# Performance work log

Hardware: AMD Instinct MI355X
Metric: run time of the kernel (lower is better)

Reference implementation:

```python
import jax, jax.numpy as jnp
import numpy as np

V, F_IN, H, DH, T = 512, 8, 64, 4, 3
E, P, L = 8192, 64, 8
D = H + DH  # path-decoder GRU width


def setup_inputs() -> dict:
    key = jax.random.key(0)
    ks = jax.random.split(key, 24)
    s = 0.1
    inp = {
        "adj_matrix": jax.random.normal(ks[0], (V, V, F_IN), jnp.float32),
        "edges": jax.random.randint(ks[1], (E, 2), 0, V),
        "paths": jax.random.randint(ks[2], (P, L), 0, V),
        "demands": jax.random.uniform(ks[3], (P,), jnp.float32),
        "emb_w": jax.random.normal(ks[4], (H, F_IN), jnp.float32) * s,
        "w1s": jax.random.normal(ks[5], (T, H, H), jnp.float32) * s,
        "w2s": jax.random.normal(ks[6], (T, H, H), jnp.float32) * s,
        "w3s": jax.random.normal(ks[7], (T, H, H), jnp.float32) * s,
        "gru_w_ih": jax.random.normal(ks[8], (3 * H, 2 * H), jnp.float32) * s,
        "gru_w_hh": jax.random.normal(ks[9], (3 * H, H), jnp.float32) * s,
        "gru_b_ih": jax.random.normal(ks[10], (3 * H,), jnp.float32) * s,
        "gru_b_hh": jax.random.normal(ks[11], (3 * H,), jnp.float32) * s,
        "pf_w_ih": jax.random.normal(ks[12], (3 * D, D), jnp.float32) * s,
        "pf_w_hh": jax.random.normal(ks[13], (3 * D, D), jnp.float32) * s,
        "pf_b_ih": jax.random.normal(ks[14], (3 * D,), jnp.float32) * s,
        "pf_b_hh": jax.random.normal(ks[15], (3 * D,), jnp.float32) * s,
        "pb_w_ih": jax.random.normal(ks[16], (3 * D, D), jnp.float32) * s,
        "pb_w_hh": jax.random.normal(ks[17], (3 * D, D), jnp.float32) * s,
        "pb_b_ih": jax.random.normal(ks[18], (3 * D,), jnp.float32) * s,
        "pb_b_hh": jax.random.normal(ks[19], (3 * D,), jnp.float32) * s,
        "wq": jax.random.normal(ks[20], (1, D), jnp.float32) * s,
        "bq": jax.random.normal(ks[21], (1,), jnp.float32) * s,
        "wd": jax.random.normal(ks[22], (DH, 1), jnp.float32) * s,
    }
    return inp


def _gru(x_seq, h0, w_ih, w_hh, b_ih, b_hh):
    """torch-style GRU, batch_first. x_seq (B,Tn,I), h0 (B,Hd) -> (ys, h_last)."""
    def step(h, x_t):
        gi = x_t @ w_ih.T + b_ih
        gh = h @ w_hh.T + b_hh
        ir, iz, inn = jnp.split(gi, 3, axis=-1)
        hr, hz, hn = jnp.split(gh, 3, axis=-1)
        r = jax.nn.sigmoid(ir + hr)
        z = jax.nn.sigmoid(iz + hz)
        n = jnp.tanh(inn + r * hn)
        h_new = (1.0 - z) * n + z * h
        return h_new, h_new
    h_last, ys = jax.lax.scan(step, h0, jnp.swapaxes(x_seq, 0, 1))
    return jnp.swapaxes(ys, 0, 1), h_last


def _message_passing(x, u, v, w1, w2, w3):
    """Vectorized form of the per-edge python loop. x (V,V,Hd), u/v (E,)."""
    Hd = x.shape[-1]
    col_sum = x.sum(axis=0)                      # (V,Hd): sum over first index
    nz_row = jnp.sum(x != 0, axis=-1)            # (V,V) nonzero count per entry
    col_nz = nz_row.sum(axis=0)                  # (V,)
    # incoming edges for edge (u,v): column u, row v zeroed, mean over nonzeros
    s_in = col_sum[u] - x[v, u]                  # (E,Hd)
    n_in = (col_nz[u] - nz_row[v, u]).astype(x.dtype) / Hd
    n_in = jnp.where(n_in == 0, 1.0, n_in)
    e_in = s_in / n_in[:, None]
    # outgoing edges: reversed edge (v,u) -> column v, row u zeroed
    s_out = col_sum[v] - x[u, v]
    n_out = (col_nz[v] - nz_row[u, v]).astype(x.dtype) / Hd
    n_out = jnp.where(n_out == 0, 1.0, n_out)
    e_out = s_out / n_out[:, None]
    m = jax.nn.relu(x[u, v] @ w1.T + e_in @ w2.T + e_out @ w3.T)
    return x.at[u, v].set(m)


def reference(adj_matrix, edges, paths, demands, emb_w, w1s, w2s, w3s,
              gru_w_ih, gru_w_hh, gru_b_ih, gru_b_hh,
              pf_w_ih, pf_w_hh, pf_b_ih, pf_b_hh,
              pb_w_ih, pb_w_hh, pb_b_ih, pb_b_hh, wq, bq, wd):
    u, v = edges[:, 0], edges[:, 1]
    x = adj_matrix @ emb_w.T                     # (V,V,H)
    for t in range(T):
        m = _message_passing(x, u, v, w1s[t], w2s[t], w3s[t])
        inp = jnp.concatenate([m, x], axis=-1)   # (V,V,2H)
        x, _ = _gru(inp, jnp.zeros((x.shape[0], H), x.dtype),
                    gru_w_ih, gru_w_hh, gru_b_ih, gru_b_hh)
    demand_emb = jax.nn.relu(demands[:, None] @ wd.T)        # (P,DH)
    graph_emb = jnp.concatenate([x.mean(axis=(0, 1)),
                                 jnp.zeros((DH,), x.dtype)])  # (D,)
    src, dst = paths[:, :-1], paths[:, 1:]                    # (P,L-1)
    edge_feat = x[src, dst]                                   # (P,L-1,H)
    dem = jnp.broadcast_to(demand_emb[:, None, :], (P, L - 1, DH))
    feat = jnp.concatenate([edge_feat, dem], axis=-1)         # (P,L-1,D)
    h0 = jnp.broadcast_to(graph_emb, (P, D))
    _, hf = _gru(feat, h0, pf_w_ih, pf_w_hh, pf_b_ih, pf_b_hh)
    _, hb = _gru(feat[:, ::-1], h0, pb_w_ih, pb_w_hh, pb_b_ih, pb_b_hh)
    paths_emb = (hf + hb) * 0.5                               # mean over directions
    return jax.nn.softmax(paths_emb @ wq.T + bq, axis=0)      # (P,1)
```

## Files before the change

kernel.cpp:

```cpp
#include <hip/hip_runtime.h>


__device__ __forceinline__ float fsig_(float x) { return 1.f / (1.f + __expf(-x)); }
__device__ __forceinline__ float ftanh_(float x) {
  float e = __expf(2.f * x);
  return 1.f - 2.f / (e + 1.f);
}
__device__ __forceinline__ float sig_(float x) { return 1.f / (1.f + expf(-x)); }

__device__ __forceinline__ void barrier_lgkm() {
  asm volatile("s_waitcnt lgkmcnt(0)\n\ts_barrier" ::: "memory");
}

#define PIN4(v) asm volatile("" : "+v"((v).x), "+v"((v).y), "+v"((v).z), "+v"((v).w))

#define LD4(p) (*(const float4*)(p))
#define DOT4(acc, va, vb)                                                      \
  do {                                                                         \
    acc += (va).x * (vb).x; acc += (va).y * (vb).y;                            \
    acc += (va).z * (vb).z; acc += (va).w * (vb).w;                            \
  } while (0)

#define ALL16(M) M(0) M(1) M(2) M(3) M(4) M(5) M(6) M(7)                       \
                 M(8) M(9) M(10) M(11) M(12) M(13) M(14) M(15)
#define ALLQ(M) M(0,0) M(1,1) M(2,2) M(3,3) M(4,0) M(5,1) M(6,2) M(7,3)        \
                M(8,0) M(9,1) M(10,2) M(11,3) M(12,0) M(13,1) M(14,2) M(15,3)

__global__ __launch_bounds__(256) void embed_kernel(
    const float* __restrict__ adj, const float* __restrict__ emb,
    float* __restrict__ x)
{
  const int64_t row = (int64_t)blockIdx.x * 4 + (threadIdx.x >> 6);
  const int h = threadIdx.x & 63;
  const float* a = adj + row * 8;
  float acc = 0.f;
#pragma unroll
  for (int f = 0; f < 8; ++f) acc += a[f] * emb[h * 8 + f];
  x[row * 64 + h] = acc;
}

__global__ __launch_bounds__(256) void colsum_kernel(
    const float* __restrict__ x, float* __restrict__ col_sum,
    int* __restrict__ col_nz)
{
  const int j = blockIdx.x;
  const int h = threadIdx.x & 63;
  const int w = threadIdx.x >> 6;
  float acc = 0.f;
  int nz = 0;
  for (int i = w; i < 512; i += 4) {
    float v = x[((int64_t)i * 512 + j) * 64 + h];
    acc += v;
    nz += (v != 0.f) ? 1 : 0;
  }
  __shared__ float pacc[4][64];
  __shared__ int pnz[4];
#pragma unroll
  for (int off = 32; off > 0; off >>= 1) nz += __shfl_down(nz, off, 64);
  if (h == 0) pnz[w] = nz;
  pacc[w][h] = acc;
  __syncthreads();
  if (w == 0) {
    col_sum[j * 64 + h] = pacc[0][h] + pacc[1][h] + pacc[2][h] + pacc[3][h];
    if (h == 0) col_nz[j] = pnz[0] + pnz[1] + pnz[2] + pnz[3];
  }
}

__global__ void scatter_idx_kernel(const int* __restrict__ edges,
                                   int* __restrict__ idxmap)
{
  const int e = blockIdx.x * 256 + threadIdx.x;
  if (e < 8192) idxmap[edges[e * 2] * 512 + edges[e * 2 + 1]] = e;
}

__global__ __launch_bounds__(64) void edge_kernel(
    const float* __restrict__ x, const int* __restrict__ edges,
    const float* __restrict__ col_sum, const int* __restrict__ col_nz,
    const float* __restrict__ w1, const float* __restrict__ w2,
    const float* __restrict__ w3, const float* __restrict__ w_ih,
    float* __restrict__ delta_gi)
{
  const int e = blockIdx.x;
  const int h = threadIdx.x;
  const int u = edges[e * 2 + 0];
  const int v = edges[e * 2 + 1];
  __shared__ __align__(16) float xuv[64], ein[64], eout[64], dm[64];
  const float xuvh = x[((int64_t)u * 512 + v) * 64 + h];
  const float xvuh = x[((int64_t)v * 512 + u) * 64 + h];
  xuv[h] = xuvh;
  const int nz_vu = __popcll(__ballot(xvuh != 0.f));
  const int nz_uv = __popcll(__ballot(xuvh != 0.f));
  float n_in = (float)(col_nz[u] - nz_vu) / 64.f;
  if (n_in == 0.f) n_in = 1.f;
  float n_out = (float)(col_nz[v] - nz_uv) / 64.f;
  if (n_out == 0.f) n_out = 1.f;
  ein[h] = (col_sum[u * 64 + h] - xvuh) / n_in;
  eout[h] = (col_sum[v * 64 + h] - xuvh) / n_out;
  __syncthreads();
  const float4* w1r = (const float4*)(w1 + h * 64);
  const float4* w2r = (const float4*)(w2 + h * 64);
  const float4* w3r = (const float4*)(w3 + h * 64);
  const float4* xuv4 = (const float4*)xuv;
  const float4* ein4 = (const float4*)ein;
  const float4* eout4 = (const float4*)eout;
  float acc = 0.f;
#pragma unroll
  for (int kk = 0; kk < 16; ++kk) {
    float4 a = xuv4[kk], b = w1r[kk];
    acc += a.x * b.x + a.y * b.y + a.z * b.z + a.w * b.w;
    a = ein4[kk]; b = w2r[kk];
    acc += a.x * b.x + a.y * b.y + a.z * b.z + a.w * b.w;
    a = eout4[kk]; b = w3r[kk];
    acc += a.x * b.x + a.y * b.y + a.z * b.z + a.w * b.w;
  }
  const float m = fmaxf(acc, 0.f);
  dm[h] = m - xuvh;
  __syncthreads();
  const float4* dm4 = (const float4*)dm;
#pragma unroll
  for (int r = 0; r < 3; ++r) {
    const int gg = h + r * 64;
    const float4* wr = (const float4*)(w_ih + gg * 128);
    float d = 0.f;
#pragma unroll
    for (int kk = 0; kk < 16; ++kk) {
      float4 a = dm4[kk], b = wr[kk];
      d += a.x * b.x + a.y * b.y + a.z * b.z + a.w * b.w;
    }
    delta_gi[e * 192 + gg] = d;
  }
}

#define DECL_W(i)                                                              \
  float4 W##i; {                                                               \
    float4 t0 = LD4(wg + 4 * (i));                                             \
    float4 t1 = LD4(wg + 64 + 4 * (i));                                        \
    W##i.x = t0.x + t1.x; W##i.y = t0.y + t1.y;                                \
    W##i.z = t0.z + t1.z; W##i.w = t0.w + t1.w;                                \
  }                                                                            \
  PIN4(W##i);
#define DECL_X(i) float4 X##i = LD4(xrow + 4 * (i));
#define PQ(i, q) { DOT4(ac##q, X##i, W##i); X##i = LD4(xnext + 4 * (i)); }
#define DECL_WR(i) float4 WR##i = LD4(wr_ + 4 * (i)); PIN4(WR##i);
#define DECL_WZ(i) float4 WZ##i = LD4(wz_ + 4 * (i)); PIN4(WZ##i);
#define DECL_WN(i) float4 WN##i = LD4(wn_ + 4 * (i)); PIN4(WN##i);
#define CCHUNK(i)                                                              \
  { float4 hc = hs4[(i)];                                                      \
    DOT4(racc, hc, WR##i); DOT4(zacc, hc, WZ##i); DOT4(nacc, hc, WN##i); }

__global__ __launch_bounds__(512, 1) void scan_kernel(
    float* __restrict__ x, const float* __restrict__ delta_gi,
    const int* __restrict__ idxmap,
    const float* __restrict__ w_ih, const float* __restrict__ w_hh,
    const float* __restrict__ b_ih, const float* __restrict__ b_hh)
{
  const int tid = threadIdx.x;
  const int wave = tid >> 6;
  const int lane = tid & 63;
  const int row = tid >> 8;
  const int b = blockIdx.x * 2 + row;
  const bool isCons = (wave == 2) || (wave == 7);

  __shared__ __align__(16) float hs[2][64];
  __shared__ float gib[2][2][192];
  __shared__ int idxl[2][512];
  float* xrow = x + (int64_t)b * 32768;

  for (int i = (tid & 255); i < 512; i += 256) idxl[row][i] = idxmap[b * 512 + i];

  if (!isCons) {
    const int pw = row ? (wave - 4) : (wave - (wave == 3));
    const int g = pw * 64 + lane;
    const float* wg = w_ih + g * 128;
    ALL16(DECL_W)
    const float bi = b_ih[g];
    ALL16(DECL_X)
    __syncthreads();
    {
      float ac0 = bi, ac1 = 0.f, ac2 = 0.f, ac3 = 0.f;
      const float* xnext = xrow + 64;
      ALLQ(PQ)
      float acc = (ac0 + ac1) + (ac2 + ac3);
      const int i0 = idxl[row][0];
      if (i0 >= 0) acc += delta_gi[(int64_t)i0 * 192 + g];
      gib[row][0][g] = acc;
    }
    const int idx1 = idxl[row][1];
    float dgn = 0.f;
    if (idx1 >= 0) dgn = delta_gi[(int64_t)idx1 * 192 + g];
    barrier_lgkm();
    for (int t = 0; t < 512; ++t) {
      if (t < 511) {
        const int tn2 = (t + 2 < 512) ? (t + 2) : 511;
        const float* xnext = xrow + tn2 * 64;
        float ac0 = bi + dgn, ac1 = 0.f, ac2 = 0.f, ac3 = 0.f;
        ALLQ(PQ)
        gib[row][(t + 1) & 1][g] = (ac0 + ac1) + (ac2 + ac3);
        const int idxn = idxl[row][tn2];
        dgn = 0.f;
        if (idxn >= 0) dgn = delta_gi[(int64_t)idxn * 192 + g];
      }
      barrier_lgkm();
    }
  } else {
    const int j = lane;
    const float* wr_ = w_hh + j * 64;
    const float* wz_ = w_hh + (j + 64) * 64;
    const float* wn_ = w_hh + (j + 128) * 64;
    ALL16(DECL_WR)
    ALL16(DECL_WZ)
    ALL16(DECL_WN)
    const float bhr = b_hh[j], bhz = b_hh[j + 64], bhn = b_hh[j + 128];
    float hj = 0.f;
    hs[row][j] = 0.f;
    __syncthreads();
    __builtin_amdgcn_s_setprio(1);
    barrier_lgkm();
    const float4* hs4 = (const float4*)hs[row];
    for (int t = 0; t < 512; ++t) {
      const float gr = gib[row][t & 1][j];
      const float gz = gib[row][t & 1][64 + j];
      const float gn = gib[row][t & 1][128 + j];
      float racc = bhr, zacc = bhz, nacc = bhn;
      ALL16(CCHUNK)
      const float r = fsig_(gr + racc);
      const float z = fsig_(gz + zacc);
      const float n = ftanh_(gn + r * nacc);
      hj = (1.f - z) * n + z * hj;
      hs[row][j] = hj;
      xrow[t * 64 + j] = hj;
      barrier_lgkm();
    }
  }
}

__global__ __launch_bounds__(64) void graphemb_kernel(
    const float* __restrict__ col_sum, float* __restrict__ graph_emb)
{
  const int h = threadIdx.x;
  float s = 0.f;
#pragma unroll 8
  for (int j = 0; j < 512; ++j) s += col_sum[j * 64 + h];
  graph_emb[h] = s * (1.f / 262144.f);
  if (h < 4) graph_emb[64 + h] = 0.f;
}

__global__ __launch_bounds__(256) void path_kernel(
    const float* __restrict__ x, const int* __restrict__ paths,
    const float* __restrict__ demands, const float* __restrict__ wd,
    const float* __restrict__ graph_emb,
    const float* __restrict__ wih_f, const float* __restrict__ whh_f,
    const float* __restrict__ bih_f, const float* __restrict__ bhh_f,
    const float* __restrict__ wih_b, const float* __restrict__ whh_b,
    const float* __restrict__ bih_b, const float* __restrict__ bhh_b,
    float* __restrict__ h_out)
{
  const int p = blockIdx.x & 63;
  const int dir = blockIdx.x >> 6;
  const int g = threadIdx.x;
  const float* w_ih = dir ? wih_b : wih_f;
  const float* w_hh = dir ? whh_b : whh_f;
  const float* bih = dir ? bih_b : bih_f;
  const float* bhh = dir ? bhh_b : bhh_f;
  __shared__ float feat[7][68], hs[68], rbuf[68], zbuf[68];
  if (g < 68) {
#pragma unroll
    for (int t = 0; t < 7; ++t) {
      const int src = paths[p * 8 + t];
      const int dst = paths[p * 8 + t + 1];
      feat[t][g] = (g < 64) ? x[((int64_t)src * 512 + dst) * 64 + g]
                            : fmaxf(demands[p] * wd[g - 64], 0.f);
    }
    hs[g] = graph_emb[g];
  }
  __syncthreads();
  for (int s = 0; s < 7; ++s) {
    const int t = dir ? (6 - s) : s;
    float acc = 0.f, hacc = 0.f;
    if (g < 204) {
      acc = bih[g];
      hacc = bhh[g];
      for (int k = 0; k < 68; ++k) {
        acc += feat[t][k] * w_ih[g * 68 + k];
        hacc += hs[k] * w_hh[g * 68 + k];
      }
    }
    if (g < 68) rbuf[g] = sig_(acc + hacc);
    else if (g < 136) zbuf[g - 68] = sig_(acc + hacc);
    __syncthreads();
    if (g >= 136 && g < 204) {
      const int j = g - 136;
      const float n = tanhf(acc + rbuf[j] * hacc);
      const float z = zbuf[j];
      const float hn = (1.f - z) * n + z * hs[j];
      hs[j] = hn;
    }
    __syncthreads();
  }
  if (g < 68) h_out[(dir * 64 + p) * 68 + g] = hs[g];
}

__global__ __launch_bounds__(64) void combine_kernel(
    const float* __restrict__ h_out, const float* __restrict__ wq,
    const float* __restrict__ bq, float* __restrict__ out)
{
  const int p = threadIdx.x;
  float l = bq[0];
#pragma unroll
  for (int d = 0; d < 68; ++d)
    l += 0.5f * (h_out[p * 68 + d] + h_out[(64 + p) * 68 + d]) * wq[d];
  float mx = l;
#pragma unroll
  for (int off = 32; off > 0; off >>= 1) mx = fmaxf(mx, __shfl_xor(mx, off, 64));
  const float e = expf(l - mx);
  float s = e;
#pragma unroll
  for (int off = 32; off > 0; off >>= 1) s += __shfl_xor(s, off, 64);
  out[p] = e / s;
}

extern "C" void kernel_launch(void* const* d_in, const int* in_sizes, int n_in,
                              void* d_out, int out_size, void* d_ws, size_t ws_size,
                              hipStream_t stream)
{
  const float* adj = (const float*)d_in[0];
  const int* edges = (const int*)d_in[1];
  const int* paths = (const int*)d_in[2];
  const float* demands = (const float*)d_in[3];
  const float* emb_w = (const float*)d_in[4];
  const float* w1s = (const float*)d_in[5];
  const float* w2s = (const float*)d_in[6];
  const float* w3s = (const float*)d_in[7];
  const float* gru_w_ih = (const float*)d_in[8];
  const float* gru_w_hh = (const float*)d_in[9];
  const float* gru_b_ih = (const float*)d_in[10];
  const float* gru_b_hh = (const float*)d_in[11];
  const float* pf_w_ih = (const float*)d_in[12];
  const float* pf_w_hh = (const float*)d_in[13];
  const float* pf_b_ih = (const float*)d_in[14];
  const float* pf_b_hh = (const float*)d_in[15];
  const float* pb_w_ih = (const float*)d_in[16];
  const float* pb_w_hh = (const float*)d_in[17];
  const float* pb_b_ih = (const float*)d_in[18];
  const float* pb_b_hh = (const float*)d_in[19];
  const float* wq = (const float*)d_in[20];
  const float* bq = (const float*)d_in[21];
  const float* wd = (const float*)d_in[22];
  float* out = (float*)d_out;

  float* xA = (float*)d_ws;
  float* col_sum = xA + 16777216;
  int* col_nz = (int*)(col_sum + 32768);
  int* idxmap = col_nz + 512;
  float* delta_gi = (float*)(idxmap + 262144);
  float* graph_emb = delta_gi + 1572864;
  float* h_out = graph_emb + 128;

  hipMemsetAsync(idxmap, 0xFF, 262144 * sizeof(int), stream);
  scatter_idx_kernel<<<32, 256, 0, stream>>>(edges, idxmap);
  embed_kernel<<<65536, 256, 0, stream>>>(adj, emb_w, xA);

  for (int t = 0; t < 3; ++t) {
    colsum_kernel<<<512, 256, 0, stream>>>(xA, col_sum, col_nz);
    edge_kernel<<<8192, 64, 0, stream>>>(xA, edges, col_sum, col_nz,
        w1s + t * 4096, w2s + t * 4096, w3s + t * 4096, gru_w_ih, delta_gi);
    scan_kernel<<<256, 512, 0, stream>>>(xA, delta_gi, idxmap,
        gru_w_ih, gru_w_hh, gru_b_ih, gru_b_hh);
  }

  colsum_kernel<<<512, 256, 0, stream>>>(xA, col_sum, col_nz);
  graphemb_kernel<<<1, 64, 0, stream>>>(col_sum, graph_emb);
  path_kernel<<<128, 256, 0, stream>>>(xA, paths, demands, wd, graph_emb,
      pf_w_ih, pf_w_hh, pf_b_ih, pf_b_hh,
      pb_w_ih, pb_w_hh, pb_b_ih, pb_b_hh, h_out);
  combine_kernel<<<1, 64, 0, stream>>>(h_out, wq, bq, out);
}
```

Baseline: 2.076 ms.

## Split GRU scan gates across waves and k-halves with two-barrier step

```diff
diff --git a/kernel.cpp b/kernel.cpp
--- a/kernel.cpp
+++ b/kernel.cpp
@@ -25,6 +25,8 @@
                  M(8) M(9) M(10) M(11) M(12) M(13) M(14) M(15)
 #define ALLQ(M) M(0,0) M(1,1) M(2,2) M(3,3) M(4,0) M(5,1) M(6,2) M(7,3)        \
                 M(8,0) M(9,1) M(10,2) M(11,3) M(12,0) M(13,1) M(14,2) M(15,3)
+#define ALL8(M) M(0) M(1) M(2) M(3) M(4) M(5) M(6) M(7)
+#define ALLQ8(M) M(0,0) M(1,1) M(2,2) M(3,3) M(4,0) M(5,1) M(6,2) M(7,3)
 
 __global__ __launch_bounds__(256) void embed_kernel(
     const float* __restrict__ adj, const float* __restrict__ emb,
@@ -131,24 +133,22 @@
   }
 }
 
-#define DECL_W(i)                                                              \
-  float4 W##i; {                                                               \
+#define DECL_WP(i)                                                             \
+  float4 WP##i; {                                                              \
     float4 t0 = LD4(wg + 4 * (i));                                             \
-    float4 t1 = LD4(wg + 64 + 4 * (i));                                        \
-    W##i.x = t0.x + t1.x; W##i.y = t0.y + t1.y;                                \
-    W##i.z = t0.z + t1.z; W##i.w = t0.w + t1.w;                                \
+    float4 t1 = LD4(wg2 + 4 * (i));                                            \
+    WP##i.x = t0.x + t1.x; WP##i.y = t0.y + t1.y;                              \
+    WP##i.z = t0.z + t1.z; WP##i.w = t0.w + t1.w;                              \
   }                                                                            \
-  PIN4(W##i);
-#define DECL_X(i) float4 X##i = LD4(xrow + 4 * (i));
-#define PQ(i, q) { DOT4(ac##q, X##i, W##i); X##i = LD4(xnext + 4 * (i)); }
-#define DECL_WR(i) float4 WR##i = LD4(wr_ + 4 * (i)); PIN4(WR##i);
-#define DECL_WZ(i) float4 WZ##i = LD4(wz_ + 4 * (i)); PIN4(WZ##i);
-#define DECL_WN(i) float4 WN##i = LD4(wn_ + 4 * (i)); PIN4(WN##i);
-#define CCHUNK(i)                                                              \
-  { float4 hc = hs4[(i)];                                                      \
-    DOT4(racc, hc, WR##i); DOT4(zacc, hc, WZ##i); DOT4(nacc, hc, WN##i); }
-
-__global__ __launch_bounds__(512, 1) void scan_kernel(
+  PIN4(WP##i);
+#define DECL_XA(i) float4 XA##i = LD4(xpA + 4 * (i));
+#define DECL_XB(i) float4 XB##i = LD4(xpB + 4 * (i));
+#define PQA(i, q) { DOT4(ac##q, XA##i, WP##i); XA##i = LD4(xnext + 4 * (i)); }
+#define PQB(i, q) { DOT4(ac##q, XB##i, WP##i); XB##i = LD4(xnext + 4 * (i)); }
+#define DECL_WC(i) float4 WC##i = LD4(wc + 4 * (i)); PIN4(WC##i);
+#define CCH(i, q) { float4 hc = hs4[(i)]; DOT4(a##q, hc, WC##i); }
+
+__global__ __launch_bounds__(768, 3) void scan_kernel(
     float* __restrict__ x, const float* __restrict__ delta_gi,
     const int* __restrict__ idxmap,
     const float* __restrict__ w_ih, const float* __restrict__ w_hh,
@@ -157,78 +157,119 @@
   const int tid = threadIdx.x;
   const int wave = tid >> 6;
   const int lane = tid & 63;
-  const int row = tid >> 8;
-  const int b = blockIdx.x * 2 + row;
-  const bool isCons = (wave == 2) || (wave == 7);
-
+  const int64_t b0 = (int64_t)blockIdx.x * 2;
+
+  __shared__ float gpart[2][2][2][192];
   __shared__ __align__(16) float hs[2][64];
-  __shared__ float gib[2][2][192];
+  __shared__ float rbuf[2][64], zbuf[2][64];
   __shared__ int idxl[2][512];
-  float* xrow = x + (int64_t)b * 32768;
-
-  for (int i = (tid & 255); i < 512; i += 256) idxl[row][i] = idxmap[b * 512 + i];
-
-  if (!isCons) {
-    const int pw = row ? (wave - 4) : (wave - (wave == 3));
-    const int g = pw * 64 + lane;
-    const float* wg = w_ih + g * 128;
-    ALL16(DECL_W)
-    const float bi = b_ih[g];
-    ALL16(DECL_X)
-    __syncthreads();
+
+  for (int i = tid; i < 1024; i += 768) {
+    const int r_ = i >> 9, ii = i & 511;
+    idxl[r_][ii] = idxmap[(b0 + r_) * 512 + ii];
+  }
+  if (tid < 128) hs[tid >> 6][tid & 63] = 0.f;
+  __syncthreads();
+
+  if (wave >= 6) {
+    const int pidx = wave - 6;
+    const int gg = pidx >> 1, khalf = pidx & 1;
+    const int g = gg * 64 + lane;
+    const float* wg = w_ih + g * 128 + khalf * 32;
+    const float* wg2 = wg + 64;
+    ALL8(DECL_WP)
+    const float bi = khalf ? 0.f : b_ih[g];
+    float* xrowA = x + b0 * 32768;
+    float* xrowB = xrowA + 32768;
+    const float* xpA = xrowA + khalf * 32;
+    const float* xpB = xrowB + khalf * 32;
+    ALL8(DECL_XA)
+    ALL8(DECL_XB)
     {
+      const float* xnext = xrowA + 64 + khalf * 32;
       float ac0 = bi, ac1 = 0.f, ac2 = 0.f, ac3 = 0.f;
-      const float* xnext = xrow + 64;
-      ALLQ(PQ)
+      ALLQ8(PQA)
       float acc = (ac0 + ac1) + (ac2 + ac3);
-      const int i0 = idxl[row][0];
-      if (i0 >= 0) acc += delta_gi[(int64_t)i0 * 192 + g];
-      gib[row][0][g] = acc;
-    }
-    const int idx1 = idxl[row][1];
-    float dgn = 0.f;
-    if (idx1 >= 0) dgn = delta_gi[(int64_t)idx1 * 192 + g];
+      if (!khalf) {
+        const int i0 = idxl[0][0];
+        if (i0 >= 0) acc += delta_gi[(int64_t)i0 * 192 + g];
+      }
+      gpart[0][0][khalf][g] = acc;
+    }
+    {
+      const float* xnext = xrowB + 64 + khalf * 32;
+      float ac0 = bi, ac1 = 0.f, ac2 = 0.f, ac3 = 0.f;
+      ALLQ8(PQB)
+      float acc = (ac0 + ac1) + (ac2 + ac3);
+      if (!khalf) {
+        const int i0 = idxl[1][0];
+        if (i0 >= 0) acc += delta_gi[(int64_t)i0 * 192 + g];
+      }
+      gpart[1][0][khalf][g] = acc;
+    }
+    float dgnA = 0.f, dgnB = 0.f;
+    if (!khalf) {
+      const int iA = idxl[0][1];
+      if (iA >= 0) dgnA = delta_gi[(int64_t)iA * 192 + g];
+      const int iB = idxl[1][1];
+      if (iB >= 0) dgnB = delta_gi[(int64_t)iB * 192 + g];
+    }
     barrier_lgkm();
     for (int t = 0; t < 512; ++t) {
       if (t < 511) {
-        const int tn2 = (t + 2 < 512) ? (t + 2) : 511;
-        const float* xnext = xrow + tn2 * 64;
-        float ac0 = bi + dgn, ac1 = 0.f, ac2 = 0.f, ac3 = 0.f;
-        ALLQ(PQ)
-        gib[row][(t + 1) & 1][g] = (ac0 + ac1) + (ac2 + ac3);
-        const int idxn = idxl[row][tn2];
-        dgn = 0.f;
-        if (idxn >= 0) dgn = delta_gi[(int64_t)idxn * 192 + g];
+        const int tn2 = (t + 2 < 512) ? t + 2 : 511;
+        {
+          const float* xnext = xrowA + tn2 * 64 + khalf * 32;
+          float ac0 = bi + dgnA, ac1 = 0.f, ac2 = 0.f, ac3 = 0.f;
+          ALLQ8(PQA)
+          gpart[0][(t + 1) & 1][khalf][g] = (ac0 + ac1) + (ac2 + ac3);
+        }
+        {
+          const float* xnext = xrowB + tn2 * 64 + khalf * 32;
+          float ac0 = bi + dgnB, ac1 = 0.f, ac2 = 0.f, ac3 = 0.f;
+          ALLQ8(PQB)
+          gpart[1][(t + 1) & 1][khalf][g] = (ac0 + ac1) + (ac2 + ac3);
+        }
+        if (!khalf) {
+          const int iA = idxl[0][tn2];
+          dgnA = (iA >= 0) ? delta_gi[(int64_t)iA * 192 + g] : 0.f;
+          const int iB = idxl[1][tn2];
+          dgnB = (iB >= 0) ? delta_gi[(int64_t)iB * 192 + g] : 0.f;
+        }
       }
       barrier_lgkm();
+      barrier_lgkm();
     }
   } else {
+    const int row = wave / 3;
+    const int cw = wave - row * 3;
     const int j = lane;
-    const float* wr_ = w_hh + j * 64;
-    const float* wz_ = w_hh + (j + 64) * 64;
-    const float* wn_ = w_hh + (j + 128) * 64;
-    ALL16(DECL_WR)
-    ALL16(DECL_WZ)
-    ALL16(DECL_WN)
-    const float bhr = b_hh[j], bhz = b_hh[j + 64], bhn = b_hh[j + 128];
-    float hj = 0.f;
-    hs[row][j] = 0.f;
-    __syncthreads();
+    const float* wc = w_hh + (cw * 64 + j) * 64;
+    ALL16(DECL_WC)
+    const float bc = b_hh[cw * 64 + j];
+    float* xrow = x + (b0 + row) * 32768;
     __builtin_amdgcn_s_setprio(1);
     barrier_lgkm();
     const float4* hs4 = (const float4*)hs[row];
+    float hj = 0.f;
     for (int t = 0; t < 512; ++t) {
-      const float gr = gib[row][t & 1][j];
-      const float gz = gib[row][t & 1][64 + j];
-      const float gn = gib[row][t & 1][128 + j];
-      float racc = bhr, zacc = bhz, nacc = bhn;
-      ALL16(CCHUNK)
-      const float r = fsig_(gr + racc);
-      const float z = fsig_(gz + zacc);
-      const float n = ftanh_(gn + r * nacc);
-      hj = (1.f - z) * n + z * hj;
-      hs[row][j] = hj;
-      xrow[t * 64 + j] = hj;
+      const int bs = t & 1;
+      const float gp = gpart[row][bs][0][cw * 64 + j] +
+                       gpart[row][bs][1][cw * 64 + j];
+      float a0 = bc, a1 = 0.f, a2 = 0.f, a3 = 0.f;
+      ALLQ(CCH)
+      const float hacc = (a0 + a1) + (a2 + a3);
+      if (cw == 0) rbuf[row][j] = fsig_(gp + hacc);
+      else if (cw == 1) zbuf[row][j] = fsig_(gp + hacc);
+      barrier_lgkm();
+      if (cw == 2) {
+        const float r = rbuf[row][j];
+        const float z = zbuf[row][j];
+        const float n = ftanh_(gp + r * hacc);
+        hj = (1.f - z) * n + z * hj;
+        hs[row][j] = hj;
+        xrow[t * 64 + j] = hj;
+      }
       barrier_lgkm();
     }
   }
@@ -364,7 +405,7 @@
     colsum_kernel<<<512, 256, 0, stream>>>(xA, col_sum, col_nz);
     edge_kernel<<<8192, 64, 0, stream>>>(xA, edges, col_sum, col_nz,
         w1s + t * 4096, w2s + t * 4096, w3s + t * 4096, gru_w_ih, delta_gi);
-    scan_kernel<<<256, 512, 0, stream>>>(xA, delta_gi, idxmap,
+    scan_kernel<<<256, 768, 0, stream>>>(xA, delta_gi, idxmap,
         gru_w_ih, gru_w_hh, gru_b_ih, gru_b_hh);
   }
 
```

Result: slower. 2.231 ms (+7.5%).
